# Kernel tuning notes

Measured on AMD Instinct MI355X. Metric: run time of the kernel, lower is better.

Reference implementation:

```python
import jax, jax.numpy as jnp
import numpy as np

C = 1024          # channels
H = 8             # num_channels (heads)
D = C // H        # channel_dim
POS = 16          # pos_dim (hard-coded in module)
MAX_FREQ = 16.0
MIN_FREQ = 1.0
HALF_S = 16       # samples_per_dim=32 -> offsets -16..16 -> S=33
S = 2 * HALF_S + 1


def setup_inputs() -> dict:
    key = jax.random.key(0)
    ks = jax.random.split(key, 8)
    B, L = 2, 2048
    s = 0.02  # realistic small init scale for learned weights
    return {
        "x": jax.random.normal(ks[0], (B, L, C), jnp.float32),
        "w_wave": jax.random.normal(ks[1], (3 * H, C), jnp.float32) * s,
        "b_wave": jnp.zeros((3 * H,), jnp.float32),
        "w_query": jax.random.normal(ks[2], (H * POS, C), jnp.float32) * s,
        "b_query": jnp.zeros((H * POS,), jnp.float32),
        "w_key": jax.random.normal(ks[3], (POS,), jnp.float32) * s,  # key_proj: Linear(1, POS, bias=False)
        "w_out": jax.random.normal(ks[4], (C, C), jnp.float32) * s,
        "w_se1": jax.random.normal(ks[5], (C // 4, C), jnp.float32) * s,
        "b_se1": jnp.zeros((C // 4,), jnp.float32),
        "w_se2": jax.random.normal(ks[6], (C, C // 4), jnp.float32) * s,
        "b_se2": jnp.zeros((C,), jnp.float32),
    }


def reference(x, w_wave, b_wave, w_query, b_query, w_key, w_out, w_se1, b_se1, w_se2, b_se2):
    B, L, Cc = x.shape
    offsets = jnp.arange(-HALF_S, HALF_S + 1, dtype=jnp.float32)  # stride_grid[:, 0], (S,)

    # wave params -> per-token, per-head freq / phase / decay
    wp = jax.nn.silu(x @ w_wave.T + b_wave).reshape(B, L, 3, H).transpose(0, 1, 3, 2)  # (B,L,H,3)
    freq = jax.nn.sigmoid(wp[..., 0]) * (MAX_FREQ - MIN_FREQ) + MIN_FREQ  # (B,L,H)
    phase = jnp.tanh(wp[..., 1]) * MAX_FREQ                               # (B,L,H)
    decay = jax.nn.sigmoid(wp[..., 2]) * 9.5 + 0.5                        # (B,L,H)
    freq_avg = freq.mean(axis=2)   # (B,L)
    phase_avg = phase.mean(axis=2) # (B,L)

    # learned fractional sample positions along the sequence
    centers = jnp.arange(L, dtype=jnp.float32)
    sample_pos = (centers[None, :, None]
                  + offsets[None, None, :] * freq_avg[..., None]
                  + phase_avg[..., None])                                 # (B,L,S)
    valid = (sample_pos >= 0) & (sample_pos < L)                          # (B,L,S)
    idx = jnp.clip(sample_pos.astype(jnp.int32), 0, L - 1)

    # dynamic gather of values at computed indices: (B,L,S,C)
    values = jax.vmap(lambda xf, i: xf[i])(x, idx)
    values = values.reshape(B, L, S, H, D).transpose(0, 1, 3, 2, 4)       # (B,L,H,S,D)

    queries = jax.nn.silu(x @ w_query.T + b_query).reshape(B, L, H, POS)  # (B,L,H,POS)
    rel_dist = jnp.abs(jnp.abs(offsets)[None, None, None, :] * freq[..., None])  # (B,L,H,S)
    keys = rel_dist[..., None] * w_key                                    # (B,L,H,S,POS)

    logits = jnp.einsum('blhd,blhsd->blhs', queries, keys) * (POS ** -0.5)
    vmask = valid[:, :, None, :]                                          # (B,L,1,S) -> broadcast (B,L,H,S)
    logits = jnp.where(vmask, logits, -jnp.inf)
    envelope = jnp.exp(-rel_dist / jnp.clip(decay[..., None], 0.1, None))

    attn = jax.nn.softmax(logits, axis=-1) * envelope * vmask
    attn = attn / (attn.sum(axis=-1, keepdims=True) + 1e-8)

    out = jnp.einsum('blhsd,blhs->blhd', values, attn).reshape(B, L, Cc)

    # SE-style channel gating
    se = jax.nn.sigmoid(jax.nn.silu(out @ w_se1.T + b_se1) @ w_se2.T + b_se2)
    out = (out * se) @ w_out.T                                            # (B,L,C) (spatial=(L,))

    entropy = -(attn * jnp.log(attn + 1e-8)).sum(axis=-1).mean()
    return out, -entropy
```

## Files before the change

### kernel.cpp

```cpp
#include <hip/hip_runtime.h>

typedef unsigned short u16;
typedef unsigned int u32;
typedef __attribute__((ext_vector_type(8))) __bf16 bf16x8;
typedef __attribute__((ext_vector_type(4))) float f32x4;

#define L_SEQ 2048
#define NROWS 4096
#define NHEAD 8
#define SWIN 33

__device__ __forceinline__ u16 f2b(float f) {
  u32 u = __float_as_uint(f);
  u += 0x7fffu + ((u >> 16) & 1u);
  return (u16)(u >> 16);
}
__device__ __forceinline__ float b2f(u32 lo16) { return __uint_as_float(lo16 << 16); }

__device__ __forceinline__ float sigmoidf_(float x) { return 1.f / (1.f + expf(-x)); }
__device__ __forceinline__ float siluf_(float x) { return x / (1.f + expf(-x)); }

__device__ __forceinline__ void gload_lds16(void* g, void* l) {
  __builtin_amdgcn_global_load_lds((__attribute__((address_space(1))) void*)g,
                                   (__attribute__((address_space(3))) void*)l, 16, 0, 0);
}

__global__ __launch_bounds__(256) void convert_w_kernel(
    const float* __restrict__ wq, const float* __restrict__ w1,
    const float* __restrict__ w2, const float* __restrict__ wo,
    u16* __restrict__ wqb, u16* __restrict__ w1b, u16* __restrict__ w2b,
    u16* __restrict__ wob) {
  size_t i = (size_t)blockIdx.x * 256 + threadIdx.x;
  const float* src;
  u16* dst;
  if (i < 32768) { src = wq; dst = wqb; }
  else if ((i -= 32768) < 65536) { src = w1; dst = w1b; }
  else if ((i -= 65536) < 65536) { src = w2; dst = w2b; }
  else if ((i -= 65536) < 262144) { src = wo; dst = wob; }
  else return;
  const float4 v = *(const float4*)(src + i * 4);
  uint2 pk;
  pk.x = (u32)f2b(v.x) | ((u32)f2b(v.y) << 16);
  pk.y = (u32)f2b(v.z) | ((u32)f2b(v.w) << 16);
  *(uint2*)(dst + i * 4) = pk;
}

#define RPB 8
__global__ __launch_bounds__(256) void wave_params_kernel(
    const float* __restrict__ x, const float* __restrict__ w_wave,
    const float* __restrict__ b_wave, float* __restrict__ params,
    u16* __restrict__ xb) {
  __shared__ float xs[RPB][1024];
  __shared__ float wp[RPB][24];
  const int t = threadIdx.x;
  const int row0 = blockIdx.x * RPB;
  const float4* xv = (const float4*)(x + (size_t)row0 * 1024);
  float4* xsv = (float4*)&xs[0][0];
  uint2* xbv = (uint2*)(xb + (size_t)row0 * 1024);
#pragma unroll
  for (int i = 0; i < RPB; ++i) {
    const float4 v = xv[t + 256 * i];
    xsv[t + 256 * i] = v;
    uint2 pk;
    pk.x = (u32)f2b(v.x) | ((u32)f2b(v.y) << 16);
    pk.y = (u32)f2b(v.z) | ((u32)f2b(v.w) << 16);
    xbv[t + 256 * i] = pk;
  }
  __syncthreads();
  const int wv = t >> 6, lane = t & 63;
#pragma unroll
  for (int oi = 0; oi < 6; ++oi) {
    const int o = wv * 6 + oi;
    float w[16];
#pragma unroll
    for (int k = 0; k < 16; ++k) w[k] = w_wave[o * 1024 + lane + 64 * k];
    const float bo = b_wave[o];
    for (int r = 0; r < RPB; ++r) {
      float d = 0.f;
#pragma unroll
      for (int k = 0; k < 16; ++k) d += w[k] * xs[r][lane + 64 * k];
#pragma unroll
      for (int off = 32; off; off >>= 1) d += __shfl_xor(d, off);
      if (lane == 0) wp[r][o] = siluf_(d + bo);
    }
  }
  __syncthreads();
  if (t < RPB * 8) {
    const int r = t >> 3, h = t & 7;
    float* pr = params + (size_t)(row0 + r) * 18;
    pr[h] = sigmoidf_(wp[r][h]) * 15.f + 1.f;
    pr[8 + h] = sigmoidf_(wp[r][16 + h]) * 9.5f + 0.5f;
  }
  if (t < RPB) {
    float fs = 0.f, ps = 0.f;
    for (int h = 0; h < 8; ++h) {
      fs += sigmoidf_(wp[t][h]);
      ps += tanhf(wp[t][8 + h]);
    }
    float* pr = params + (size_t)(row0 + t) * 18;
    pr[16] = fs * (15.f / 8.f) + 1.f;
    pr[17] = ps * (16.f / 8.f);
  }
}

template <int MODE, int TM, int TN, int BK>
__global__ __launch_bounds__(256) void gemm_bt(
    const u16* __restrict__ A, const u16* __restrict__ Bw,
    const float* __restrict__ bias, const u16* __restrict__ aux,
    void* __restrict__ outp, int N, int K) {
  __shared__ __align__(16) u16 As[TM * BK];
  __shared__ __align__(16) u16 Bs[TN * BK];
  const int t = threadIdx.x;
  const int bm = blockIdx.x, bn = blockIdx.y;
  constexpr int TPR = BK / 8;
  constexpr int RPP = 256 / TPR;
  const int rowS = t / TPR;
  const int colX = ((t & (TPR - 1)) ^ (rowS & (TPR - 1))) * 8;
  const u16* Ag = A + (size_t)(bm * TM + rowS) * K + colX;
  const u16* Bg = Bw + (size_t)(bn * TN + rowS) * K + colX;
  constexpr int NI = TM / 32, NJ = TN / 32;
  f32x4 acc[NI][NJ] = {};
  const int lane = t & 63, wv = t >> 6;
  const int wm = (wv >> 1) * (TM / 2);
  const int wn = (wv & 1) * (TN / 2);
  const int frow = lane & 15, quad = lane >> 4;
  for (int kt = 0; kt < K; kt += BK) {
    __syncthreads();
#pragma unroll
    for (int r = 0; r < TM; r += RPP)
      gload_lds16((void*)(Ag + kt + (size_t)r * K), (char*)As + r * BK * 2 + t * 16);
#pragma unroll
    for (int r = 0; r < TN; r += RPP)
      gload_lds16((void*)(Bg + kt + (size_t)r * K), (char*)Bs + r * BK * 2 + t * 16);
    __syncthreads();
#pragma unroll
    for (int kk = 0; kk < BK; kk += 32) {
      bf16x8 af[NI], bfr[NJ];
#pragma unroll
      for (int i = 0; i < NI; ++i) {
        const int rr = wm + i * 16 + frow;
        af[i] = *(bf16x8*)&As[rr * BK + ((((kk >> 3) + quad) ^ (rr & (TPR - 1))) * 8)];
      }
#pragma unroll
      for (int j = 0; j < NJ; ++j) {
        const int rr = wn + j * 16 + frow;
        bfr[j] = *(bf16x8*)&Bs[rr * BK + ((((kk >> 3) + quad) ^ (rr & (TPR - 1))) * 8)];
      }
#pragma unroll
      for (int i = 0; i < NI; ++i)
#pragma unroll
        for (int j = 0; j < NJ; ++j)
          acc[i][j] = __builtin_amdgcn_mfma_f32_16x16x32_bf16(af[i], bfr[j], acc[i][j], 0, 0, 0);
    }
  }
#pragma unroll
  for (int i = 0; i < NI; ++i)
#pragma unroll
    for (int j = 0; j < NJ; ++j)
#pragma unroll
      for (int r = 0; r < 4; ++r) {
        const int gm = bm * TM + wm + i * 16 + quad * 4 + r;
        const int gn = bn * TN + wn + j * 16 + frow;
        float v = acc[i][j][r];
        const size_t o = (size_t)gm * N + gn;
        if (MODE == 0) { v = siluf_(v + bias[gn]); ((float*)outp)[o] = v; }
        if (MODE == 1) { v = siluf_(v + bias[gn]); ((u16*)outp)[o] = f2b(v); }
        if (MODE == 2) { v = sigmoidf_(v + bias[gn]) * b2f(aux[o]); ((u16*)outp)[o] = f2b(v); }
        if (MODE == 3) { ((float*)outp)[o] = v; }
      }
}

__global__ __launch_bounds__(256, 2) void attn_kernel(
    const u16* __restrict__ xb, const float* __restrict__ params,
    const float* __restrict__ qbuf, const float* __restrict__ w_key,
    u16* __restrict__ outb, float* __restrict__ entpart) {
  __shared__ float qs[128];
  __shared__ float wk[16];
  __shared__ float pf[18];
  __shared__ float qkL[8];
  __shared__ int idxL[SWIN];
  __shared__ int validL[SWIN];
  __shared__ float attnL[NHEAD][SWIN];
  __shared__ float entL[8];
  const int t = threadIdx.x;
  const int bx = blockIdx.x;
  const int row = ((bx & 7) << 9) | (bx >> 3);
  const int b = row >> 11, l = row & 2047;
  if (t < 128) qs[t] = qbuf[(size_t)row * 128 + t];
  if (t < 16) wk[t] = w_key[t];
  if (t >= 128 && t < 146) pf[t - 128] = params[(size_t)row * 18 + (t - 128)];
  __syncthreads();
  if (t < SWIN) {
    const float pos = (float)l + (float)(t - 16) * pf[16] + pf[17];
    validL[t] = (pos >= 0.f) && (pos < (float)L_SEQ);
    int id = (int)pos;
    idxL[t] = min(max(id, 0), L_SEQ - 1);
  }
  if (t >= 64 && t < 72) {
    const int h = t - 64;
    float s = 0.f;
#pragma unroll
    for (int p = 0; p < 16; ++p) s += qs[h * 16 + p] * wk[p];
    qkL[h] = s * 0.25f;
  }
  __syncthreads();
  const int wv = t >> 6, lane = t & 63;
#pragma unroll
  for (int it = 0; it < 2; ++it) {
    const int h = wv + 4 * it;
    const bool act = lane < SWIN;
    const int s = act ? lane : 0;
    const float rel = fabsf((float)(s - 16)) * pf[h];
    const float logit = rel * qkL[h];
    const bool vs = act && validL[s];
    float m = vs ? logit : -INFINITY;
#pragma unroll
    for (int o = 32; o; o >>= 1) m = fmaxf(m, __shfl_xor(m, o));
    float p = vs ? expf(logit - m) : 0.f;
    float sm = p;
#pragma unroll
    for (int o = 32; o; o >>= 1) sm += __shfl_xor(sm, o);
    const float soft = sm > 0.f ? p / sm : 0.f;
    const float env = expf(-rel / fmaxf(pf[8 + h], 0.1f));
    float a = soft * env;
    float as = a;
#pragma unroll
    for (int o = 32; o; o >>= 1) as += __shfl_xor(as, o);
    a = a / (as + 1e-8f);
    if (act) attnL[h][s] = a;
    float et = a * logf(a + 1e-8f);
#pragma unroll
    for (int o = 32; o; o >>= 1) et += __shfl_xor(et, o);
    if (lane == 0) entL[h] = et;
  }
  __syncthreads();
  if (t == 0) {
    float e = 0.f;
    for (int h = 0; h < 8; ++h) e += entL[h];
    entpart[bx] = e * (1.f / 32768.f);
  }
  const u16* xbase = xb + (size_t)b * L_SEQ * 1024 + 4 * t;
  const int h = t >> 5;
  float4 acc = make_float4(0.f, 0.f, 0.f, 0.f);
  uint2 v0[11], v1[11], v2[11];
  auto LD = [&](uint2* v, int c) {
#pragma unroll
    for (int k = 0; k < 11; ++k)
      v[k] = *(const uint2*)(xbase + (size_t)idxL[c * 11 + k] * 1024);
  };
  auto FM = [&](uint2* v, int c) {
#pragma unroll
    for (int k = 0; k < 11; ++k) {
      const float a_ = attnL[h][c * 11 + k];
      acc.x += a_ * b2f(v[k].x & 0xffffu);
      acc.y += a_ * b2f(v[k].x >> 16);
      acc.z += a_ * b2f(v[k].y & 0xffffu);
      acc.w += a_ * b2f(v[k].y >> 16);
    }
  };
  LD(v0, 0); __builtin_amdgcn_sched_barrier(0);
  LD(v1, 1); __builtin_amdgcn_sched_barrier(0);
  FM(v0, 0); __builtin_amdgcn_sched_barrier(0);
  LD(v2, 2); __builtin_amdgcn_sched_barrier(0);
  FM(v1, 1); __builtin_amdgcn_sched_barrier(0);
  FM(v2, 2);
  const size_t o4 = (size_t)row * 1024 + 4 * t;
  uint2 pk;
  pk.x = (u32)f2b(acc.x) | ((u32)f2b(acc.y) << 16);
  pk.y = (u32)f2b(acc.z) | ((u32)f2b(acc.w) << 16);
  *(uint2*)(outb + o4) = pk;
}

__global__ __launch_bounds__(256) void ent_reduce_kernel(
    const float* __restrict__ entpart, float* __restrict__ entslot) {
  __shared__ float ws_[4];
  const int t = threadIdx.x;
  float s = 0.f;
#pragma unroll
  for (int i = 0; i < 16; ++i) s += entpart[t + 256 * i];
#pragma unroll
  for (int o = 32; o; o >>= 1) s += __shfl_xor(s, o);
  if ((t & 63) == 0) ws_[t >> 6] = s;
  __syncthreads();
  if (t == 0) *entslot = ws_[0] + ws_[1] + ws_[2] + ws_[3];
}

extern "C" void kernel_launch(void* const* d_in, const int* in_sizes, int n_in,
                              void* d_out, int out_size, void* d_ws, size_t ws_size,
                              hipStream_t stream) {
  const float* x = (const float*)d_in[0];
  const float* w_wave = (const float*)d_in[1];
  const float* b_wave = (const float*)d_in[2];
  const float* w_query = (const float*)d_in[3];
  const float* b_query = (const float*)d_in[4];
  const float* w_key = (const float*)d_in[5];
  const float* w_out = (const float*)d_in[6];
  const float* w_se1 = (const float*)d_in[7];
  const float* b_se1 = (const float*)d_in[8];
  const float* w_se2 = (const float*)d_in[9];
  const float* b_se2 = (const float*)d_in[10];
  float* out = (float*)d_out;
  char* ws = (char*)d_ws;
  size_t off = 0;
  auto alloc = [&](size_t bytes) { void* p = ws + off; off += (bytes + 255) & ~(size_t)255; return p; };
  float* params = (float*)alloc(NROWS * 18 * 4);
  float* qbuf = (float*)alloc((size_t)NROWS * 128 * 4);
  float* entpart = (float*)alloc(NROWS * 4);
  u16* outb = (u16*)alloc((size_t)NROWS * 1024 * 2);
  u16* t1b = (u16*)alloc((size_t)NROWS * 256 * 2);
  u16* gb = (u16*)alloc((size_t)NROWS * 1024 * 2);
  u16* xb = (u16*)alloc((size_t)NROWS * 1024 * 2);
  u16* wqb = (u16*)alloc(128 * 1024 * 2);
  u16* w1b = (u16*)alloc(256 * 1024 * 2);
  u16* w2b = (u16*)alloc(1024 * 256 * 2);
  u16* wob = (u16*)alloc((size_t)1024 * 1024 * 2);
  float* entslot = out + (out_size - 1);

  convert_w_kernel<<<dim3(1664), 256, 0, stream>>>(w_query, w_se1, w_se2, w_out,
                                                   wqb, w1b, w2b, wob);
  wave_params_kernel<<<dim3(NROWS / RPB), 256, 0, stream>>>(x, w_wave, b_wave, params, xb);
  gemm_bt<0, 64, 32, 64><<<dim3(64, 4), 256, 0, stream>>>(xb, wqb, b_query, nullptr, qbuf, 128, 1024);
  attn_kernel<<<dim3(NROWS), 256, 0, stream>>>(xb, params, qbuf, w_key, outb, entpart);
  ent_reduce_kernel<<<dim3(1), 256, 0, stream>>>(entpart, entslot);
  gemm_bt<1, 64, 64, 64><<<dim3(64, 4), 256, 0, stream>>>(outb, w1b, b_se1, nullptr, t1b, 256, 1024);
  gemm_bt<2, 128, 128, 64><<<dim3(32, 8), 256, 0, stream>>>(t1b, w2b, b_se2, outb, gb, 1024, 256);
  gemm_bt<3, 128, 128, 64><<<dim3(32, 8), 256, 0, stream>>>(gb, wob, nullptr, nullptr, out, 1024, 1024);
}
```

Baseline: 199.7 us.

## Double-buffer GEMM LDS tiles, merge weight conversion, shrink GEMM tiles

```diff
diff --git a/kernel.cpp b/kernel.cpp
--- a/kernel.cpp
+++ b/kernel.cpp
@@ -25,35 +25,36 @@
                                    (__attribute__((address_space(3))) void*)l, 16, 0, 0);
 }
 
-__global__ __launch_bounds__(256) void convert_w_kernel(
+#define RPB 8
+__global__ __launch_bounds__(256) void wave_params_kernel(
+    const float* __restrict__ x, const float* __restrict__ w_wave,
+    const float* __restrict__ b_wave, float* __restrict__ params,
+    u16* __restrict__ xb,
     const float* __restrict__ wq, const float* __restrict__ w1,
     const float* __restrict__ w2, const float* __restrict__ wo,
     u16* __restrict__ wqb, u16* __restrict__ w1b, u16* __restrict__ w2b,
     u16* __restrict__ wob) {
-  size_t i = (size_t)blockIdx.x * 256 + threadIdx.x;
-  const float* src;
-  u16* dst;
-  if (i < 32768) { src = wq; dst = wqb; }
-  else if ((i -= 32768) < 65536) { src = w1; dst = w1b; }
-  else if ((i -= 65536) < 65536) { src = w2; dst = w2b; }
-  else if ((i -= 65536) < 262144) { src = wo; dst = wob; }
-  else return;
-  const float4 v = *(const float4*)(src + i * 4);
-  uint2 pk;
-  pk.x = (u32)f2b(v.x) | ((u32)f2b(v.y) << 16);
-  pk.y = (u32)f2b(v.z) | ((u32)f2b(v.w) << 16);
-  *(uint2*)(dst + i * 4) = pk;
-}
-
-#define RPB 8
-__global__ __launch_bounds__(256) void wave_params_kernel(
-    const float* __restrict__ x, const float* __restrict__ w_wave,
-    const float* __restrict__ b_wave, float* __restrict__ params,
-    u16* __restrict__ xb) {
   __shared__ float xs[RPB][1024];
   __shared__ float wp[RPB][24];
   const int t = threadIdx.x;
-  const int row0 = blockIdx.x * RPB;
+  const int bx = blockIdx.x;
+  if (bx >= 512) {
+    size_t i = (size_t)(bx - 512) * 256 + t;
+    const float* src;
+    u16* dst;
+    if (i < 32768) { src = wq; dst = wqb; }
+    else if ((i -= 32768) < 65536) { src = w1; dst = w1b; }
+    else if ((i -= 65536) < 65536) { src = w2; dst = w2b; }
+    else if ((i -= 65536) < 262144) { src = wo; dst = wob; }
+    else return;
+    const float4 v = *(const float4*)(src + i * 4);
+    uint2 pk;
+    pk.x = (u32)f2b(v.x) | ((u32)f2b(v.y) << 16);
+    pk.y = (u32)f2b(v.z) | ((u32)f2b(v.w) << 16);
+    *(uint2*)(dst + i * 4) = pk;
+    return;
+  }
+  const int row0 = bx * RPB;
   const float4* xv = (const float4*)(x + (size_t)row0 * 1024);
   float4* xsv = (float4*)&xs[0][0];
   uint2* xbv = (uint2*)(xb + (size_t)row0 * 1024);
@@ -108,8 +109,8 @@
     const u16* __restrict__ A, const u16* __restrict__ Bw,
     const float* __restrict__ bias, const u16* __restrict__ aux,
     void* __restrict__ outp, int N, int K) {
-  __shared__ __align__(16) u16 As[TM * BK];
-  __shared__ __align__(16) u16 Bs[TN * BK];
+  __shared__ __align__(16) u16 As[2 * TM * BK];
+  __shared__ __align__(16) u16 Bs[2 * TN * BK];
   const int t = threadIdx.x;
   const int bm = blockIdx.x, bn = blockIdx.y;
   constexpr int TPR = BK / 8;
@@ -124,27 +125,33 @@
   const int wm = (wv >> 1) * (TM / 2);
   const int wn = (wv & 1) * (TN / 2);
   const int frow = lane & 15, quad = lane >> 4;
-  for (int kt = 0; kt < K; kt += BK) {
+  auto stage = [&](int buf, int kt) {
+    char* Ab = (char*)As + buf * (TM * BK * 2);
+    char* Bb = (char*)Bs + buf * (TN * BK * 2);
+#pragma unroll
+    for (int r = 0; r < TM; r += RPP)
+      gload_lds16((void*)(Ag + kt + (size_t)r * K), Ab + r * BK * 2 + t * 16);
+#pragma unroll
+    for (int r = 0; r < TN; r += RPP)
+      gload_lds16((void*)(Bg + kt + (size_t)r * K), Bb + r * BK * 2 + t * 16);
+  };
+  stage(0, 0);
+  int pb = 0;
+  for (int kt = 0; kt < K; kt += BK, pb ^= 1) {
     __syncthreads();
-#pragma unroll
-    for (int r = 0; r < TM; r += RPP)
-      gload_lds16((void*)(Ag + kt + (size_t)r * K), (char*)As + r * BK * 2 + t * 16);
-#pragma unroll
-    for (int r = 0; r < TN; r += RPP)
-      gload_lds16((void*)(Bg + kt + (size_t)r * K), (char*)Bs + r * BK * 2 + t * 16);
-    __syncthreads();
+    if (kt + BK < K) stage(pb ^ 1, kt + BK);
 #pragma unroll
     for (int kk = 0; kk < BK; kk += 32) {
       bf16x8 af[NI], bfr[NJ];
 #pragma unroll
       for (int i = 0; i < NI; ++i) {
         const int rr = wm + i * 16 + frow;
-        af[i] = *(bf16x8*)&As[rr * BK + ((((kk >> 3) + quad) ^ (rr & (TPR - 1))) * 8)];
+        af[i] = *(bf16x8*)&As[pb * TM * BK + rr * BK + ((((kk >> 3) + quad) ^ (rr & (TPR - 1))) * 8)];
       }
 #pragma unroll
       for (int j = 0; j < NJ; ++j) {
         const int rr = wn + j * 16 + frow;
-        bfr[j] = *(bf16x8*)&Bs[rr * BK + ((((kk >> 3) + quad) ^ (rr & (TPR - 1))) * 8)];
+        bfr[j] = *(bf16x8*)&Bs[pb * TN * BK + rr * BK + ((((kk >> 3) + quad) ^ (rr & (TPR - 1))) * 8)];
       }
 #pragma unroll
       for (int i = 0; i < NI; ++i)
@@ -316,13 +323,12 @@
   u16* wob = (u16*)alloc((size_t)1024 * 1024 * 2);
   float* entslot = out + (out_size - 1);
 
-  convert_w_kernel<<<dim3(1664), 256, 0, stream>>>(w_query, w_se1, w_se2, w_out,
-                                                   wqb, w1b, w2b, wob);
-  wave_params_kernel<<<dim3(NROWS / RPB), 256, 0, stream>>>(x, w_wave, b_wave, params, xb);
+  wave_params_kernel<<<dim3(512 + 1664), 256, 0, stream>>>(
+      x, w_wave, b_wave, params, xb, w_query, w_se1, w_se2, w_out, wqb, w1b, w2b, wob);
   gemm_bt<0, 64, 32, 64><<<dim3(64, 4), 256, 0, stream>>>(xb, wqb, b_query, nullptr, qbuf, 128, 1024);
   attn_kernel<<<dim3(NROWS), 256, 0, stream>>>(xb, params, qbuf, w_key, outb, entpart);
   ent_reduce_kernel<<<dim3(1), 256, 0, stream>>>(entpart, entslot);
-  gemm_bt<1, 64, 64, 64><<<dim3(64, 4), 256, 0, stream>>>(outb, w1b, b_se1, nullptr, t1b, 256, 1024);
-  gemm_bt<2, 128, 128, 64><<<dim3(32, 8), 256, 0, stream>>>(t1b, w2b, b_se2, outb, gb, 1024, 256);
-  gemm_bt<3, 128, 128, 64><<<dim3(32, 8), 256, 0, stream>>>(gb, wob, nullptr, nullptr, out, 1024, 1024);
-}
+  gemm_bt<1, 64, 32, 64><<<dim3(64, 8), 256, 0, stream>>>(outb, w1b, b_se1, nullptr, t1b, 256, 1024);
+  gemm_bt<2, 128, 64, 64><<<dim3(32, 16), 256, 0, stream>>>(t1b, w2b, b_se2, outb, gb, 1024, 256);
+  gemm_bt<3, 128, 64, 64><<<dim3(32, 16), 256, 0, stream>>>(gb, wob, nullptr, nullptr, out, 1024, 1024);
+}
```

Result: faster. 188.9 us (-5.4%).
